# Kernel tuning notes

Measured on AMD Instinct MI355X. Metric: run time of the kernel, lower is better.

The kernel has to match this reference:

```python
import jax, jax.numpy as jnp
import numpy as np

EPS = 1e-5  # torch LayerNorm default


def _layernorm(x, g, b):
    mu = jnp.mean(x, axis=-1, keepdims=True)
    var = jnp.mean(jnp.square(x - mu), axis=-1, keepdims=True)
    return (x - mu) * jax.lax.rsqrt(var + EPS) * g + b


def _sparse_window_attn(x, wq, wk, wv, wo, span, stride, head_num):
    B, L, D = x.shape
    d = D // head_num  # dim_QK == dim_V == dim_q // head_num
    Q = (x @ wq.T).reshape(B, L, head_num, d).transpose(0, 2, 1, 3)  # [B,H,L,d]
    K = (x @ wk.T).reshape(B, L, head_num, d).transpose(0, 2, 1, 3)
    V = (x @ wv.T).reshape(B, L, head_num, d).transpose(0, 2, 1, 3)
    s = jnp.arange(span)
    i = jnp.arange(L)
    kvi = s[:, None] - (span - 1) + stride * i[None, :]       # [S,L] key index per (offset, query)
    valid = (kvi >= 0) & (kvi < L)
    kvic = jnp.clip(kvi, 0, L - 1)
    Kg = K[:, :, kvic, :]                                     # [B,H,S,L,d]
    scores = jnp.einsum('bhld,bhsld->bhsl', Q, Kg) / jnp.sqrt(jnp.float32(d))
    scores = jnp.where(valid[None, None], scores, -jnp.inf)
    p = jax.nn.softmax(scores, axis=2)                        # softmax over span (dim 2 in torch)
    Vg = V[:, :, kvic, :]                                     # [B,H,S,L,d]
    o = jnp.einsum('bhsl,bhsld->bhld', p, Vg)                 # invalid entries have p==0
    o = o.transpose(0, 2, 1, 3).reshape(B, L, D)
    return o @ wo.T


def setup_inputs() -> dict:
    key = jax.random.key(0)
    ks = jax.random.split(key, 8)
    B, L, D = 2, 2048, 512
    sc = 1.0 / np.sqrt(D)
    return {
        'query': jax.random.normal(ks[0], (B, L, D), jnp.float32),
        'ln_g': jnp.ones((D,), jnp.float32),
        'ln_b': jnp.zeros((D,), jnp.float32),
        'wq': jax.random.normal(ks[1], (D, D), jnp.float32) * sc,
        'wk': jax.random.normal(ks[2], (D, D), jnp.float32) * sc,
        'wv': jax.random.normal(ks[3], (D, D), jnp.float32) * sc,
        'wo': jax.random.normal(ks[4], (D, D), jnp.float32) * sc,
        'w1': jax.random.normal(ks[5], (2 * D, D), jnp.float32) * sc,
        'b1': jnp.zeros((2 * D,), jnp.float32),
        'w2': jax.random.normal(ks[6], (D, 2 * D), jnp.float32) * (1.0 / np.sqrt(2 * D)),
        'b2': jnp.zeros((D,), jnp.float32),
        'span': 64,
        'stride': 1,
        'head_num': 8,
    }


def reference(query, ln_g, ln_b, wq, wk, wv, wo, w1, b1, w2, b2, span, stride, head_num):
    # NOTE: the torch block applies the SAME LayerNorm (shared params) twice.
    x = _layernorm(query, ln_g, ln_b)
    x = _sparse_window_attn(x, wq, wk, wv, wo, span, stride, head_num)
    query = x + query
    x = _layernorm(query, ln_g, ln_b)
    x = jax.nn.gelu(x @ w1.T + b1, approximate=False) @ w2.T + b2
    return x + query
```

## Files before the change

kernel.cpp:

```cpp
#include <hip/hip_runtime.h>
#include <hip/hip_bf16.h>
#include <cmath>

typedef __bf16 bf16;
typedef __attribute__((ext_vector_type(8))) __bf16 bf16x8;
typedef __attribute__((ext_vector_type(4))) __bf16 bf16x4;
typedef __attribute__((ext_vector_type(4))) float f32x4;
typedef __attribute__((ext_vector_type(4))) unsigned int u32x4;

#define LD_B 2
#define LD_L 2048
#define LD_D 512
#define N_HEAD 8
#define HD 64
#define NTOK (LD_B * LD_L)

__device__ __forceinline__ void gload16(const void* g, void* l) {
  __builtin_amdgcn_global_load_lds(
      (const __attribute__((address_space(1))) void*)g,
      (__attribute__((address_space(3))) void*)l, 16, 0, 0);
}

__global__ __launch_bounds__(256) void cast6_kernel(
    const float* __restrict__ s0, const float* __restrict__ s1,
    const float* __restrict__ s2, const float* __restrict__ s3,
    const float* __restrict__ s4, const float* __restrict__ s5,
    bf16* __restrict__ d0, bf16* __restrict__ d1, bf16* __restrict__ d2,
    bf16* __restrict__ d3, bf16* __restrict__ d4, bf16* __restrict__ d5)
{
  int idx = blockIdx.x * 256 + threadIdx.x;
  const float* src; bf16* dst; int off;
  if (idx < 262144) {
    int seg = idx >> 16; off = idx & 65535;
    src = seg == 0 ? s0 : seg == 1 ? s1 : seg == 2 ? s2 : s3;
    dst = seg == 0 ? d0 : seg == 1 ? d1 : seg == 2 ? d2 : d3;
  } else {
    int t = idx - 262144;
    int seg = t >> 17; off = t & 131071;
    src = seg ? s5 : s4;
    dst = seg ? d5 : d4;
  }
  f32x4 v = ((const f32x4*)src)[off];
  bf16x4 o;
  o[0] = (bf16)v[0]; o[1] = (bf16)v[1]; o[2] = (bf16)v[2]; o[3] = (bf16)v[3];
  ((bf16x4*)dst)[off] = o;
}

__global__ __launch_bounds__(256) void ln_kernel(
    const float* __restrict__ x, const float* __restrict__ g,
    const float* __restrict__ b, bf16* __restrict__ out)
{
  const int wid = threadIdx.x >> 6, lane = threadIdx.x & 63;
  const int row = blockIdx.x * 4 + wid;
  const f32x4* xr = (const f32x4*)(x + (size_t)row * LD_D);
  f32x4 v0 = xr[lane * 2], v1 = xr[lane * 2 + 1];
  float s = v0[0] + v0[1] + v0[2] + v0[3] + v1[0] + v1[1] + v1[2] + v1[3];
#pragma unroll
  for (int off = 32; off; off >>= 1) s += __shfl_xor(s, off);
  const float mu = s * (1.f / 512.f);
  float vs = 0.f;
#pragma unroll
  for (int i = 0; i < 4; ++i) {
    float a0 = v0[i] - mu; vs += a0 * a0;
    float a1 = v1[i] - mu; vs += a1 * a1;
  }
#pragma unroll
  for (int off = 32; off; off >>= 1) vs += __shfl_xor(vs, off);
  const float rstd = rsqrtf(vs * (1.f / 512.f) + 1e-5f);
  const f32x4* gr = (const f32x4*)g;
  const f32x4* br = (const f32x4*)b;
  f32x4 g0 = gr[lane * 2], g1 = gr[lane * 2 + 1];
  f32x4 b0 = br[lane * 2], b1 = br[lane * 2 + 1];
  bf16x8 o;
#pragma unroll
  for (int i = 0; i < 4; ++i) o[i] = (bf16)((v0[i] - mu) * rstd * g0[i] + b0[i]);
#pragma unroll
  for (int i = 0; i < 4; ++i) o[i + 4] = (bf16)((v1[i] - mu) * rstd * g1[i] + b1[i]);
  *(bf16x8*)(&out[(size_t)row * LD_D + lane * 8]) = o;
}

template <int EPI>
__device__ __forceinline__ void gemm_core(
    const bf16* __restrict__ A, const bf16* __restrict__ Bw,
    int M, int N, int K,
    bf16* __restrict__ Cb, float* __restrict__ Cf,
    const float* __restrict__ bias, const float* __restrict__ res)
{
  __shared__ bf16 As[2][4096];
  __shared__ bf16 Bs[2][4096];
  const int tid = threadIdx.x;
  const int lane = tid & 63, wid = tid >> 6;
  const int wm = wid >> 1, wn = wid & 1;
  const int l15 = lane & 15, kg = lane >> 4;
  const int row0 = blockIdx.x * 64, col0 = blockIdx.y * 64;

  int srow[2], scol[2];
#pragma unroll
  for (int i = 0; i < 2; ++i) {
    int c = i * 256 + tid;
    srow[i] = c >> 3;
    scol[i] = ((c & 7) ^ (srow[i] & 7)) * 8;
  }

  f32x4 acc[2][2];
#pragma unroll
  for (int m = 0; m < 2; ++m)
#pragma unroll
    for (int n = 0; n < 2; ++n) acc[m][n] = (f32x4){0.f, 0.f, 0.f, 0.f};

  const int nt = K >> 6;
#define STAGE(buf, k0)                                                      \
  {                                                                         \
    _Pragma("unroll")                                                       \
    for (int i = 0; i < 2; ++i) {                                           \
      const bf16* ga = A + (size_t)(row0 + srow[i]) * K + (k0) + scol[i];   \
      const bf16* gb = Bw + (size_t)(col0 + srow[i]) * K + (k0) + scol[i];  \
      char* la = (char*)&As[buf][0] + (i * 4 + wid) * 1024;                 \
      char* lb = (char*)&Bs[buf][0] + (i * 4 + wid) * 1024;                 \
      gload16(ga, la);                                                      \
      gload16(gb, lb);                                                      \
    }                                                                       \
  }

  STAGE(0, 0);
  __syncthreads();
  for (int t = 0; t < nt; ++t) {
    if (t + 1 < nt) STAGE((t + 1) & 1, (t + 1) << 6);
    const char* pa = (const char*)&As[t & 1][0];
    const char* pb = (const char*)&Bs[t & 1][0];
#pragma unroll
    for (int kk = 0; kk < 2; ++kk) {
      bf16x8 af[2], bf[2];
#pragma unroll
      for (int m = 0; m < 2; ++m) {
        const int r = wm * 32 + m * 16 + l15;
        int off = r * 128 + kk * 64 + kg * 16;
        off ^= (r & 7) << 4;
        af[m] = *(const bf16x8*)(pa + off);
      }
#pragma unroll
      for (int n = 0; n < 2; ++n) {
        const int r = wn * 32 + n * 16 + l15;
        int off = r * 128 + kk * 64 + kg * 16;
        off ^= (r & 7) << 4;
        bf[n] = *(const bf16x8*)(pb + off);
      }
#pragma unroll
      for (int m = 0; m < 2; ++m)
#pragma unroll
        for (int n = 0; n < 2; ++n)
          acc[m][n] = __builtin_amdgcn_mfma_f32_16x16x32_bf16(af[m], bf[n], acc[m][n], 0, 0, 0);
    }
    __syncthreads();
  }
#undef STAGE

  const int orow = row0 + wm * 32, ocol = col0 + wn * 32;
#pragma unroll
  for (int m = 0; m < 2; ++m) {
#pragma unroll
    for (int n = 0; n < 2; ++n) {
#pragma unroll
      for (int e = 0; e < 4; ++e) {
        const int rr = orow + m * 16 + kg * 4 + e;
        const int cc = ocol + n * 16 + l15;
        const float v = acc[m][n][e];
        const size_t oi = (size_t)rr * N + cc;
        if constexpr (EPI == 0) {
          Cb[oi] = (bf16)v;
        } else if constexpr (EPI == 1) {
          Cf[oi] = v + res[oi];
        } else if constexpr (EPI == 2) {
          float t = v + bias[cc];
          Cb[oi] = (bf16)(0.5f * t * (1.f + erff(t * 0.70710678118654752f)));
        } else {
          Cf[oi] = v + bias[cc] + res[oi];
        }
      }
    }
  }
}

__global__ __launch_bounds__(256) void gemm_qkv_kernel(
    const bf16* __restrict__ A, const bf16* __restrict__ Wq,
    const bf16* __restrict__ Wk, const bf16* __restrict__ Wv,
    bf16* __restrict__ Qo, bf16* __restrict__ Ko, bf16* __restrict__ Vo)
{
  const bf16* W = blockIdx.z == 0 ? Wq : blockIdx.z == 1 ? Wk : Wv;
  bf16* O = blockIdx.z == 0 ? Qo : blockIdx.z == 1 ? Ko : Vo;
  gemm_core<0>(A, W, NTOK, 512, 512, O, nullptr, nullptr, nullptr);
}

template <int EPI>
__global__ __launch_bounds__(256) void gemm_kernel(
    const bf16* __restrict__ A, const bf16* __restrict__ Bw,
    int M, int N, int K, bf16* Cb, float* Cf,
    const float* __restrict__ bias, const float* __restrict__ res)
{
  gemm_core<EPI>(A, Bw, M, N, K, Cb, Cf, bias, res);
}

__global__ __launch_bounds__(256) void attn_kernel(
    const bf16* __restrict__ Qg, const bf16* __restrict__ Kg,
    const bf16* __restrict__ Vg, bf16* __restrict__ Og)
{
  constexpr int STK = 72;
  constexpr int STP = 136;
  __shared__ bf16 Ks[128][STK];
  __shared__ bf16 Qs[64][STK];
  __shared__ bf16 Vt[64][STP];
  __shared__ bf16 Ps[4][16][STP];
  const int tid = threadIdx.x;
  const int qt = blockIdx.x, bh = blockIdx.y;
  const int b = bh >> 3, h = bh & 7;
  const int q0 = qt * 64;
  const int j0 = q0 - 63;
  const size_t base = (size_t)b * LD_L * LD_D + h * HD;

  for (int c = tid; c < 128 * 8; c += 256) {
    const int r = c >> 3, d0 = (c & 7) * 8;
    const int j = j0 + r;
    u32x4 kv = (u32x4){0u, 0u, 0u, 0u};
    bf16x8 vv = (bf16x8)(__bf16)0.f;
    if (j >= 0 && j < LD_L) {
      kv = *(const u32x4*)(Kg + base + (size_t)j * LD_D + d0);
      vv = *(const bf16x8*)(Vg + base + (size_t)j * LD_D + d0);
    }
    *(u32x4*)(&Ks[r][d0]) = kv;
#pragma unroll
    for (int dd = 0; dd < 8; ++dd) Vt[d0 + dd][r] = vv[dd];
  }
  for (int c = tid; c < 64 * 8; c += 256) {
    const int r = c >> 3, d0 = (c & 7) * 8;
    *(u32x4*)(&Qs[r][d0]) =
        *(const u32x4*)(Qg + base + (size_t)(q0 + r) * LD_D + d0);
  }
  __syncthreads();

  const int lane = tid & 63, wid = tid >> 6;
  const int l15 = lane & 15, kg = lane >> 4;
  const int klo = 63 - q0;

  bf16x8 qf[2];
#pragma unroll
  for (int kk = 0; kk < 2; ++kk)
    qf[kk] = *(const bf16x8*)(&Qs[wid * 16 + l15][kk * 32 + kg * 8]);
  f32x4 s[8];
#pragma unroll
  for (int n = 0; n < 8; ++n) s[n] = (f32x4){0.f, 0.f, 0.f, 0.f};
#pragma unroll
  for (int kk = 0; kk < 2; ++kk)
#pragma unroll
    for (int n = 0; n < 8; ++n) {
      bf16x8 kf = *(const bf16x8*)(&Ks[n * 16 + l15][kk * 32 + kg * 8]);
      s[n] = __builtin_amdgcn_mfma_f32_16x16x32_bf16(qf[kk], kf, s[n], 0, 0, 0);
    }

  float p[8][4];
  float mx[4], sm[4];
#pragma unroll
  for (int e = 0; e < 4; ++e) { mx[e] = -INFINITY; sm[e] = 0.f; }
#pragma unroll
  for (int n = 0; n < 8; ++n) {
    const int k = n * 16 + l15;
#pragma unroll
    for (int e = 0; e < 4; ++e) {
      const int qi = wid * 16 + kg * 4 + e;
      const bool ok = (k >= qi) & (k <= qi + 63) & (k >= klo);
      float sv = ok ? s[n][e] * 0.125f : -INFINITY;
      p[n][e] = sv;
      mx[e] = fmaxf(mx[e], sv);
    }
  }
#pragma unroll
  for (int off = 8; off; off >>= 1)
#pragma unroll
    for (int e = 0; e < 4; ++e) mx[e] = fmaxf(mx[e], __shfl_xor(mx[e], off));
#pragma unroll
  for (int n = 0; n < 8; ++n)
#pragma unroll
    for (int e = 0; e < 4; ++e) {
      float pv = (p[n][e] == -INFINITY) ? 0.f : __expf(p[n][e] - mx[e]);
      p[n][e] = pv;
      sm[e] += pv;
    }
#pragma unroll
  for (int off = 8; off; off >>= 1)
#pragma unroll
    for (int e = 0; e < 4; ++e) sm[e] += __shfl_xor(sm[e], off);
  float rs[4];
#pragma unroll
  for (int e = 0; e < 4; ++e) rs[e] = 1.f / sm[e];

#pragma unroll
  for (int n = 0; n < 8; ++n)
#pragma unroll
    for (int e = 0; e < 4; ++e)
      Ps[wid][kg * 4 + e][n * 16 + l15] = (bf16)(p[n][e] * rs[e]);

  f32x4 o[4];
#pragma unroll
  for (int n = 0; n < 4; ++n) o[n] = (f32x4){0.f, 0.f, 0.f, 0.f};
#pragma unroll
  for (int ks = 0; ks < 4; ++ks) {
    bf16x8 pf = *(const bf16x8*)(&Ps[wid][l15][ks * 32 + kg * 8]);
#pragma unroll
    for (int n = 0; n < 4; ++n) {
      bf16x8 vf = *(const bf16x8*)(&Vt[n * 16 + l15][ks * 32 + kg * 8]);
      o[n] = __builtin_amdgcn_mfma_f32_16x16x32_bf16(pf, vf, o[n], 0, 0, 0);
    }
  }

  const int q = q0 + wid * 16 + kg * 4;
#pragma unroll
  for (int n = 0; n < 4; ++n)
#pragma unroll
    for (int e = 0; e < 4; ++e)
      Og[base + (size_t)(q + e) * LD_D + n * 16 + l15] = (bf16)o[n][e];
}

extern "C" void kernel_launch(void* const* d_in, const int* in_sizes, int n_in,
                              void* d_out, int out_size, void* d_ws, size_t ws_size,
                              hipStream_t stream)
{
  const float* query = (const float*)d_in[0];
  const float* ln_g = (const float*)d_in[1];
  const float* ln_b = (const float*)d_in[2];
  const float* wq = (const float*)d_in[3];
  const float* wk = (const float*)d_in[4];
  const float* wv = (const float*)d_in[5];
  const float* wo = (const float*)d_in[6];
  const float* w1 = (const float*)d_in[7];
  const float* b1 = (const float*)d_in[8];
  const float* w2 = (const float*)d_in[9];
  const float* b2 = (const float*)d_in[10];
  float* out = (float*)d_out;

  char* ws = (char*)d_ws;
  bf16* WQb = (bf16*)(ws + 0x000000);
  bf16* WKb = (bf16*)(ws + 0x080000);
  bf16* WVb = (bf16*)(ws + 0x100000);
  bf16* WOb = (bf16*)(ws + 0x180000);
  bf16* W1b = (bf16*)(ws + 0x200000);
  bf16* W2b = (bf16*)(ws + 0x300000);
  bf16* XLN = (bf16*)(ws + 0x400000);
  bf16* Qb  = (bf16*)(ws + 0x800000);
  bf16* Kb  = (bf16*)(ws + 0xC00000);
  bf16* Vb  = (bf16*)(ws + 0x1000000);
  bf16* ATb = (bf16*)(ws + 0x1400000);
  float* Q2 = (float*)(ws + 0x1800000);
  bf16* YLN = (bf16*)(ws + 0x2000000);
  bf16* Hb  = (bf16*)(ws + 0x2400000);

  cast6_kernel<<<2048, 256, 0, stream>>>(wq, wk, wv, wo, w1, w2,
                                         WQb, WKb, WVb, WOb, W1b, W2b);
  ln_kernel<<<1024, 256, 0, stream>>>(query, ln_g, ln_b, XLN);
  gemm_qkv_kernel<<<dim3(64, 8, 3), 256, 0, stream>>>(XLN, WQb, WKb, WVb, Qb, Kb, Vb);
  attn_kernel<<<dim3(32, 16), 256, 0, stream>>>(Qb, Kb, Vb, ATb);
  gemm_kernel<1><<<dim3(64, 8), 256, 0, stream>>>(ATb, WOb, NTOK, 512, 512,
                                                  nullptr, Q2, nullptr, query);
  ln_kernel<<<1024, 256, 0, stream>>>(Q2, ln_g, ln_b, YLN);
  gemm_kernel<2><<<dim3(64, 16), 256, 0, stream>>>(YLN, W1b, NTOK, 1024, 512,
                                                   Hb, nullptr, b1, nullptr);
  gemm_kernel<3><<<dim3(64, 8), 256, 0, stream>>>(Hb, W2b, NTOK, 512, 1024,
                                                  nullptr, out, b2, Q2);
}
```

Measured before the change: 152.5 us.

## Fuse QKV weights into one GEMM and enlarge GEMM tiles to 128

Concatenates Wq/Wk/Wv into a single 1536-wide weight so the QKV projection runs as one GEMM writing an interleaved QKV buffer, and the attention kernel reads Q/K/V from it with a 1536 row stride. The GEMM is templated on block tile size and all projections now use 128x128 or 128x64 tiles, raising data reuse per block at the cost of more registers and LDS and fewer blocks on a large GPU.

```diff
diff --git a/kernel.cpp b/kernel.cpp
--- a/kernel.cpp
+++ b/kernel.cpp
@@ -14,6 +14,7 @@
 #define N_HEAD 8
 #define HD 64
 #define NTOK (LD_B * LD_L)
+#define QKV_LD 1536
 
 __device__ __forceinline__ void gload16(const void* g, void* l) {
   __builtin_amdgcn_global_load_lds(
@@ -79,48 +80,59 @@
   *(bf16x8*)(&out[(size_t)row * LD_D + lane * 8]) = o;
 }
 
-template <int EPI>
-__device__ __forceinline__ void gemm_core(
+template <int BM, int BN, int EPI>
+__global__ __launch_bounds__(256) void gemm_kernel(
     const bf16* __restrict__ A, const bf16* __restrict__ Bw,
-    int M, int N, int K,
-    bf16* __restrict__ Cb, float* __restrict__ Cf,
+    int M, int N, int K, bf16* __restrict__ Cb, float* __restrict__ Cf,
     const float* __restrict__ bias, const float* __restrict__ res)
 {
-  __shared__ bf16 As[2][4096];
-  __shared__ bf16 Bs[2][4096];
+  constexpr int WM = BM / 2, WN = BN / 2;
+  constexpr int FM = WM / 16, FN = WN / 16;
+  constexpr int IA = BM / 32, IB = BN / 32;
+  __shared__ bf16 As[2][BM * 64];
+  __shared__ bf16 Bs[2][BN * 64];
   const int tid = threadIdx.x;
   const int lane = tid & 63, wid = tid >> 6;
   const int wm = wid >> 1, wn = wid & 1;
   const int l15 = lane & 15, kg = lane >> 4;
-  const int row0 = blockIdx.x * 64, col0 = blockIdx.y * 64;
-
-  int srow[2], scol[2];
-#pragma unroll
-  for (int i = 0; i < 2; ++i) {
+  const int row0 = blockIdx.x * BM, col0 = blockIdx.y * BN;
+
+  int srowA[IA], scolA[IA];
+#pragma unroll
+  for (int i = 0; i < IA; ++i) {
     int c = i * 256 + tid;
-    srow[i] = c >> 3;
-    scol[i] = ((c & 7) ^ (srow[i] & 7)) * 8;
-  }
-
-  f32x4 acc[2][2];
-#pragma unroll
-  for (int m = 0; m < 2; ++m)
-#pragma unroll
-    for (int n = 0; n < 2; ++n) acc[m][n] = (f32x4){0.f, 0.f, 0.f, 0.f};
+    srowA[i] = c >> 3;
+    scolA[i] = ((c & 7) ^ (srowA[i] & 7)) * 8;
+  }
+  int srowB[IB], scolB[IB];
+#pragma unroll
+  for (int i = 0; i < IB; ++i) {
+    int c = i * 256 + tid;
+    srowB[i] = c >> 3;
+    scolB[i] = ((c & 7) ^ (srowB[i] & 7)) * 8;
+  }
+
+  f32x4 acc[FM][FN];
+#pragma unroll
+  for (int m = 0; m < FM; ++m)
+#pragma unroll
+    for (int n = 0; n < FN; ++n) acc[m][n] = (f32x4){0.f, 0.f, 0.f, 0.f};
 
   const int nt = K >> 6;
-#define STAGE(buf, k0)                                                      \
-  {                                                                         \
-    _Pragma("unroll")                                                       \
-    for (int i = 0; i < 2; ++i) {                                           \
-      const bf16* ga = A + (size_t)(row0 + srow[i]) * K + (k0) + scol[i];   \
-      const bf16* gb = Bw + (size_t)(col0 + srow[i]) * K + (k0) + scol[i];  \
-      char* la = (char*)&As[buf][0] + (i * 4 + wid) * 1024;                 \
-      char* lb = (char*)&Bs[buf][0] + (i * 4 + wid) * 1024;                 \
-      gload16(ga, la);                                                      \
-      gload16(gb, lb);                                                      \
-    }                                                                       \
-  }
+  auto STAGE = [&](int buf, int k0) {
+#pragma unroll
+    for (int i = 0; i < IA; ++i) {
+      const bf16* ga = A + (size_t)(row0 + srowA[i]) * K + k0 + scolA[i];
+      char* la = (char*)&As[buf][0] + i * 4096 + wid * 1024;
+      gload16(ga, la);
+    }
+#pragma unroll
+    for (int i = 0; i < IB; ++i) {
+      const bf16* gb = Bw + (size_t)(col0 + srowB[i]) * K + k0 + scolB[i];
+      char* lb = (char*)&Bs[buf][0] + i * 4096 + wid * 1024;
+      gload16(gb, lb);
+    }
+  };
 
   STAGE(0, 0);
   __syncthreads();
@@ -130,36 +142,35 @@
     const char* pb = (const char*)&Bs[t & 1][0];
 #pragma unroll
     for (int kk = 0; kk < 2; ++kk) {
-      bf16x8 af[2], bf[2];
-#pragma unroll
-      for (int m = 0; m < 2; ++m) {
-        const int r = wm * 32 + m * 16 + l15;
+      bf16x8 af[FM], bf[FN];
+#pragma unroll
+      for (int m = 0; m < FM; ++m) {
+        const int r = wm * WM + m * 16 + l15;
         int off = r * 128 + kk * 64 + kg * 16;
         off ^= (r & 7) << 4;
         af[m] = *(const bf16x8*)(pa + off);
       }
 #pragma unroll
-      for (int n = 0; n < 2; ++n) {
-        const int r = wn * 32 + n * 16 + l15;
+      for (int n = 0; n < FN; ++n) {
+        const int r = wn * WN + n * 16 + l15;
         int off = r * 128 + kk * 64 + kg * 16;
         off ^= (r & 7) << 4;
         bf[n] = *(const bf16x8*)(pb + off);
       }
 #pragma unroll
-      for (int m = 0; m < 2; ++m)
-#pragma unroll
-        for (int n = 0; n < 2; ++n)
+      for (int m = 0; m < FM; ++m)
+#pragma unroll
+        for (int n = 0; n < FN; ++n)
           acc[m][n] = __builtin_amdgcn_mfma_f32_16x16x32_bf16(af[m], bf[n], acc[m][n], 0, 0, 0);
     }
     __syncthreads();
   }
-#undef STAGE
-
-  const int orow = row0 + wm * 32, ocol = col0 + wn * 32;
-#pragma unroll
-  for (int m = 0; m < 2; ++m) {
-#pragma unroll
-    for (int n = 0; n < 2; ++n) {
+
+  const int orow = row0 + wm * WM, ocol = col0 + wn * WN;
+#pragma unroll
+  for (int m = 0; m < FM; ++m) {
+#pragma unroll
+    for (int n = 0; n < FN; ++n) {
 #pragma unroll
       for (int e = 0; e < 4; ++e) {
         const int rr = orow + m * 16 + kg * 4 + e;
@@ -171,8 +182,8 @@
         } else if constexpr (EPI == 1) {
           Cf[oi] = v + res[oi];
         } else if constexpr (EPI == 2) {
-          float t = v + bias[cc];
-          Cb[oi] = (bf16)(0.5f * t * (1.f + erff(t * 0.70710678118654752f)));
+          float t2 = v + bias[cc];
+          Cb[oi] = (bf16)(0.5f * t2 * (1.f + erff(t2 * 0.70710678118654752f)));
         } else {
           Cf[oi] = v + bias[cc] + res[oi];
         }
@@ -181,28 +192,8 @@
   }
 }
 
-__global__ __launch_bounds__(256) void gemm_qkv_kernel(
-    const bf16* __restrict__ A, const bf16* __restrict__ Wq,
-    const bf16* __restrict__ Wk, const bf16* __restrict__ Wv,
-    bf16* __restrict__ Qo, bf16* __restrict__ Ko, bf16* __restrict__ Vo)
-{
-  const bf16* W = blockIdx.z == 0 ? Wq : blockIdx.z == 1 ? Wk : Wv;
-  bf16* O = blockIdx.z == 0 ? Qo : blockIdx.z == 1 ? Ko : Vo;
-  gemm_core<0>(A, W, NTOK, 512, 512, O, nullptr, nullptr, nullptr);
-}
-
-template <int EPI>
-__global__ __launch_bounds__(256) void gemm_kernel(
-    const bf16* __restrict__ A, const bf16* __restrict__ Bw,
-    int M, int N, int K, bf16* Cb, float* Cf,
-    const float* __restrict__ bias, const float* __restrict__ res)
-{
-  gemm_core<EPI>(A, Bw, M, N, K, Cb, Cf, bias, res);
-}
-
 __global__ __launch_bounds__(256) void attn_kernel(
-    const bf16* __restrict__ Qg, const bf16* __restrict__ Kg,
-    const bf16* __restrict__ Vg, bf16* __restrict__ Og)
+    const bf16* __restrict__ QKV, bf16* __restrict__ Og)
 {
   constexpr int STK = 72;
   constexpr int STP = 136;
@@ -215,7 +206,10 @@
   const int b = bh >> 3, h = bh & 7;
   const int q0 = qt * 64;
   const int j0 = q0 - 63;
-  const size_t base = (size_t)b * LD_L * LD_D + h * HD;
+  const size_t baseQ = (size_t)b * LD_L * QKV_LD + h * HD;
+  const size_t baseK = baseQ + 512;
+  const size_t baseV = baseQ + 1024;
+  const size_t baseO = (size_t)b * LD_L * LD_D + h * HD;
 
   for (int c = tid; c < 128 * 8; c += 256) {
     const int r = c >> 3, d0 = (c & 7) * 8;
@@ -223,8 +217,8 @@
     u32x4 kv = (u32x4){0u, 0u, 0u, 0u};
     bf16x8 vv = (bf16x8)(__bf16)0.f;
     if (j >= 0 && j < LD_L) {
-      kv = *(const u32x4*)(Kg + base + (size_t)j * LD_D + d0);
-      vv = *(const bf16x8*)(Vg + base + (size_t)j * LD_D + d0);
+      kv = *(const u32x4*)(QKV + baseK + (size_t)j * QKV_LD + d0);
+      vv = *(const bf16x8*)(QKV + baseV + (size_t)j * QKV_LD + d0);
     }
     *(u32x4*)(&Ks[r][d0]) = kv;
 #pragma unroll
@@ -233,7 +227,7 @@
   for (int c = tid; c < 64 * 8; c += 256) {
     const int r = c >> 3, d0 = (c & 7) * 8;
     *(u32x4*)(&Qs[r][d0]) =
-        *(const u32x4*)(Qg + base + (size_t)(q0 + r) * LD_D + d0);
+        *(const u32x4*)(QKV + baseQ + (size_t)(q0 + r) * QKV_LD + d0);
   }
   __syncthreads();
 
@@ -316,7 +310,7 @@
   for (int n = 0; n < 4; ++n)
 #pragma unroll
     for (int e = 0; e < 4; ++e)
-      Og[base + (size_t)(q + e) * LD_D + n * 16 + l15] = (bf16)o[n][e];
+      Og[baseO + (size_t)(q + e) * LD_D + n * 16 + l15] = (bf16)o[n][e];
 }
 
 extern "C" void kernel_launch(void* const* d_in, const int* in_sizes, int n_in,
@@ -337,31 +331,29 @@
   float* out = (float*)d_out;
 
   char* ws = (char*)d_ws;
-  bf16* WQb = (bf16*)(ws + 0x000000);
-  bf16* WKb = (bf16*)(ws + 0x080000);
-  bf16* WVb = (bf16*)(ws + 0x100000);
+  bf16* WQKVb = (bf16*)(ws + 0x000000);
   bf16* WOb = (bf16*)(ws + 0x180000);
   bf16* W1b = (bf16*)(ws + 0x200000);
   bf16* W2b = (bf16*)(ws + 0x300000);
   bf16* XLN = (bf16*)(ws + 0x400000);
-  bf16* Qb  = (bf16*)(ws + 0x800000);
-  bf16* Kb  = (bf16*)(ws + 0xC00000);
-  bf16* Vb  = (bf16*)(ws + 0x1000000);
+  bf16* QKVb = (bf16*)(ws + 0x800000);
   bf16* ATb = (bf16*)(ws + 0x1400000);
   float* Q2 = (float*)(ws + 0x1800000);
   bf16* YLN = (bf16*)(ws + 0x2000000);
-  bf16* Hb  = (bf16*)(ws + 0x2400000);
-
-  cast6_kernel<<<2048, 256, 0, stream>>>(wq, wk, wv, wo, w1, w2,
-                                         WQb, WKb, WVb, WOb, W1b, W2b);
+  bf16* Hb = (bf16*)(ws + 0x2400000);
+
+  cast6_kernel<<<2048, 256, 0, stream>>>(
+      wq, wk, wv, wo, w1, w2,
+      WQKVb, WQKVb + 262144, WQKVb + 524288, WOb, W1b, W2b);
   ln_kernel<<<1024, 256, 0, stream>>>(query, ln_g, ln_b, XLN);
-  gemm_qkv_kernel<<<dim3(64, 8, 3), 256, 0, stream>>>(XLN, WQb, WKb, WVb, Qb, Kb, Vb);
-  attn_kernel<<<dim3(32, 16), 256, 0, stream>>>(Qb, Kb, Vb, ATb);
-  gemm_kernel<1><<<dim3(64, 8), 256, 0, stream>>>(ATb, WOb, NTOK, 512, 512,
-                                                  nullptr, Q2, nullptr, query);
+  gemm_kernel<128, 128, 0><<<dim3(32, 12), 256, 0, stream>>>(
+      XLN, WQKVb, NTOK, QKV_LD, 512, QKVb, nullptr, nullptr, nullptr);
+  attn_kernel<<<dim3(32, 16), 256, 0, stream>>>(QKVb, ATb);
+  gemm_kernel<128, 64, 1><<<dim3(32, 8), 256, 0, stream>>>(
+      ATb, WOb, NTOK, 512, 512, nullptr, Q2, nullptr, query);
   ln_kernel<<<1024, 256, 0, stream>>>(Q2, ln_g, ln_b, YLN);
-  gemm_kernel<2><<<dim3(64, 16), 256, 0, stream>>>(YLN, W1b, NTOK, 1024, 512,
-                                                   Hb, nullptr, b1, nullptr);
-  gemm_kernel<3><<<dim3(64, 8), 256, 0, stream>>>(Hb, W2b, NTOK, 512, 1024,
-                                                  nullptr, out, b2, Q2);
-}
+  gemm_kernel<128, 128, 2><<<dim3(32, 8), 256, 0, stream>>>(
+      YLN, W1b, NTOK, 1024, 512, Hb, nullptr, b1, nullptr);
+  gemm_kernel<128, 64, 3><<<dim3(32, 8), 256, 0, stream>>>(
+      Hb, W2b, NTOK, 512, 1024, nullptr, out, b2, Q2);
+}
```

Measured after the change: 161.8 us. 1.06x slower.

## Fuse weight cast with first LayerNorm and pack QKV into one GEMM

Applied to the files above, without the earlier changes.

Merges the weight-cast kernel and the first LayerNorm into a single prep kernel whose blocks are split by index, saving one launch. The Q, K and V weights are written contiguously so one GEMM with N=1536 produces an interleaved QKV buffer. The attention kernel now reads Q, K and V from that buffer with a row stride of 1536. This removes a launch and the per-block weight selection, at the cost of strided reads in attention.

```diff
diff --git a/kernel.cpp b/kernel.cpp
--- a/kernel.cpp
+++ b/kernel.cpp
@@ -14,6 +14,7 @@
 #define N_HEAD 8
 #define HD 64
 #define NTOK (LD_B * LD_L)
+#define QKV_LD 1536
 
 __device__ __forceinline__ void gload16(const void* g, void* l) {
   __builtin_amdgcn_global_load_lds(
@@ -21,35 +22,34 @@
       (__attribute__((address_space(3))) void*)l, 16, 0, 0);
 }
 
-__global__ __launch_bounds__(256) void cast6_kernel(
+__global__ __launch_bounds__(256) void prep_kernel(
+    const float* __restrict__ x, const float* __restrict__ g,
+    const float* __restrict__ b, bf16* __restrict__ xln,
     const float* __restrict__ s0, const float* __restrict__ s1,
     const float* __restrict__ s2, const float* __restrict__ s3,
     const float* __restrict__ s4, const float* __restrict__ s5,
     bf16* __restrict__ d0, bf16* __restrict__ d1, bf16* __restrict__ d2,
     bf16* __restrict__ d3, bf16* __restrict__ d4, bf16* __restrict__ d5)
 {
-  int idx = blockIdx.x * 256 + threadIdx.x;
-  const float* src; bf16* dst; int off;
-  if (idx < 262144) {
-    int seg = idx >> 16; off = idx & 65535;
-    src = seg == 0 ? s0 : seg == 1 ? s1 : seg == 2 ? s2 : s3;
-    dst = seg == 0 ? d0 : seg == 1 ? d1 : seg == 2 ? d2 : d3;
-  } else {
-    int t = idx - 262144;
-    int seg = t >> 17; off = t & 131071;
-    src = seg ? s5 : s4;
-    dst = seg ? d5 : d4;
-  }
-  f32x4 v = ((const f32x4*)src)[off];
-  bf16x4 o;
-  o[0] = (bf16)v[0]; o[1] = (bf16)v[1]; o[2] = (bf16)v[2]; o[3] = (bf16)v[3];
-  ((bf16x4*)dst)[off] = o;
-}
-
-__global__ __launch_bounds__(256) void ln_kernel(
-    const float* __restrict__ x, const float* __restrict__ g,
-    const float* __restrict__ b, bf16* __restrict__ out)
-{
+  if (blockIdx.x >= 1024) {
+    int idx = (blockIdx.x - 1024) * 256 + threadIdx.x;
+    const float* src; bf16* dst; int off;
+    if (idx < 262144) {
+      int seg = idx >> 16; off = idx & 65535;
+      src = seg == 0 ? s0 : seg == 1 ? s1 : seg == 2 ? s2 : s3;
+      dst = seg == 0 ? d0 : seg == 1 ? d1 : seg == 2 ? d2 : d3;
+    } else {
+      int t = idx - 262144;
+      int seg = t >> 17; off = t & 131071;
+      src = seg ? s5 : s4;
+      dst = seg ? d5 : d4;
+    }
+    f32x4 v = ((const f32x4*)src)[off];
+    bf16x4 o;
+    o[0] = (bf16)v[0]; o[1] = (bf16)v[1]; o[2] = (bf16)v[2]; o[3] = (bf16)v[3];
+    ((bf16x4*)dst)[off] = o;
+    return;
+  }
   const int wid = threadIdx.x >> 6, lane = threadIdx.x & 63;
   const int row = blockIdx.x * 4 + wid;
   const f32x4* xr = (const f32x4*)(x + (size_t)row * LD_D);
@@ -76,14 +76,46 @@
   for (int i = 0; i < 4; ++i) o[i] = (bf16)((v0[i] - mu) * rstd * g0[i] + b0[i]);
 #pragma unroll
   for (int i = 0; i < 4; ++i) o[i + 4] = (bf16)((v1[i] - mu) * rstd * g1[i] + b1[i]);
+  *(bf16x8*)(&xln[(size_t)row * LD_D + lane * 8]) = o;
+}
+
+__global__ __launch_bounds__(256) void ln_kernel(
+    const float* __restrict__ x, const float* __restrict__ g,
+    const float* __restrict__ b, bf16* __restrict__ out)
+{
+  const int wid = threadIdx.x >> 6, lane = threadIdx.x & 63;
+  const int row = blockIdx.x * 4 + wid;
+  const f32x4* xr = (const f32x4*)(x + (size_t)row * LD_D);
+  f32x4 v0 = xr[lane * 2], v1 = xr[lane * 2 + 1];
+  float s = v0[0] + v0[1] + v0[2] + v0[3] + v1[0] + v1[1] + v1[2] + v1[3];
+#pragma unroll
+  for (int off = 32; off; off >>= 1) s += __shfl_xor(s, off);
+  const float mu = s * (1.f / 512.f);
+  float vs = 0.f;
+#pragma unroll
+  for (int i = 0; i < 4; ++i) {
+    float a0 = v0[i] - mu; vs += a0 * a0;
+    float a1 = v1[i] - mu; vs += a1 * a1;
+  }
+#pragma unroll
+  for (int off = 32; off; off >>= 1) vs += __shfl_xor(vs, off);
+  const float rstd = rsqrtf(vs * (1.f / 512.f) + 1e-5f);
+  const f32x4* gr = (const f32x4*)g;
+  const f32x4* br = (const f32x4*)b;
+  f32x4 g0 = gr[lane * 2], g1 = gr[lane * 2 + 1];
+  f32x4 b0 = br[lane * 2], b1 = br[lane * 2 + 1];
+  bf16x8 o;
+#pragma unroll
+  for (int i = 0; i < 4; ++i) o[i] = (bf16)((v0[i] - mu) * rstd * g0[i] + b0[i]);
+#pragma unroll
+  for (int i = 0; i < 4; ++i) o[i + 4] = (bf16)((v1[i] - mu) * rstd * g1[i] + b1[i]);
   *(bf16x8*)(&out[(size_t)row * LD_D + lane * 8]) = o;
 }
 
 template <int EPI>
-__device__ __forceinline__ void gemm_core(
+__global__ __launch_bounds__(256) void gemm_kernel(
     const bf16* __restrict__ A, const bf16* __restrict__ Bw,
-    int M, int N, int K,
-    bf16* __restrict__ Cb, float* __restrict__ Cf,
+    int M, int N, int K, bf16* __restrict__ Cb, float* __restrict__ Cf,
     const float* __restrict__ bias, const float* __restrict__ res)
 {
   __shared__ bf16 As[2][4096];
@@ -171,8 +203,8 @@
         } else if constexpr (EPI == 1) {
           Cf[oi] = v + res[oi];
         } else if constexpr (EPI == 2) {
-          float t = v + bias[cc];
-          Cb[oi] = (bf16)(0.5f * t * (1.f + erff(t * 0.70710678118654752f)));
+          float t2 = v + bias[cc];
+          Cb[oi] = (bf16)(0.5f * t2 * (1.f + erff(t2 * 0.70710678118654752f)));
         } else {
           Cf[oi] = v + bias[cc] + res[oi];
         }
@@ -181,28 +213,8 @@
   }
 }
 
-__global__ __launch_bounds__(256) void gemm_qkv_kernel(
-    const bf16* __restrict__ A, const bf16* __restrict__ Wq,
-    const bf16* __restrict__ Wk, const bf16* __restrict__ Wv,
-    bf16* __restrict__ Qo, bf16* __restrict__ Ko, bf16* __restrict__ Vo)
-{
-  const bf16* W = blockIdx.z == 0 ? Wq : blockIdx.z == 1 ? Wk : Wv;
-  bf16* O = blockIdx.z == 0 ? Qo : blockIdx.z == 1 ? Ko : Vo;
-  gemm_core<0>(A, W, NTOK, 512, 512, O, nullptr, nullptr, nullptr);
-}
-
-template <int EPI>
-__global__ __launch_bounds__(256) void gemm_kernel(
-    const bf16* __restrict__ A, const bf16* __restrict__ Bw,
-    int M, int N, int K, bf16* Cb, float* Cf,
-    const float* __restrict__ bias, const float* __restrict__ res)
-{
-  gemm_core<EPI>(A, Bw, M, N, K, Cb, Cf, bias, res);
-}
-
 __global__ __launch_bounds__(256) void attn_kernel(
-    const bf16* __restrict__ Qg, const bf16* __restrict__ Kg,
-    const bf16* __restrict__ Vg, bf16* __restrict__ Og)
+    const bf16* __restrict__ QKV, bf16* __restrict__ Og)
 {
   constexpr int STK = 72;
   constexpr int STP = 136;
@@ -215,7 +227,10 @@
   const int b = bh >> 3, h = bh & 7;
   const int q0 = qt * 64;
   const int j0 = q0 - 63;
-  const size_t base = (size_t)b * LD_L * LD_D + h * HD;
+  const size_t baseQ = (size_t)b * LD_L * QKV_LD + h * HD;
+  const size_t baseK = baseQ + 512;
+  const size_t baseV = baseQ + 1024;
+  const size_t baseO = (size_t)b * LD_L * LD_D + h * HD;
 
   for (int c = tid; c < 128 * 8; c += 256) {
     const int r = c >> 3, d0 = (c & 7) * 8;
@@ -223,8 +238,8 @@
     u32x4 kv = (u32x4){0u, 0u, 0u, 0u};
     bf16x8 vv = (bf16x8)(__bf16)0.f;
     if (j >= 0 && j < LD_L) {
-      kv = *(const u32x4*)(Kg + base + (size_t)j * LD_D + d0);
-      vv = *(const bf16x8*)(Vg + base + (size_t)j * LD_D + d0);
+      kv = *(const u32x4*)(QKV + baseK + (size_t)j * QKV_LD + d0);
+      vv = *(const bf16x8*)(QKV + baseV + (size_t)j * QKV_LD + d0);
     }
     *(u32x4*)(&Ks[r][d0]) = kv;
 #pragma unroll
@@ -233,7 +248,7 @@
   for (int c = tid; c < 64 * 8; c += 256) {
     const int r = c >> 3, d0 = (c & 7) * 8;
     *(u32x4*)(&Qs[r][d0]) =
-        *(const u32x4*)(Qg + base + (size_t)(q0 + r) * LD_D + d0);
+        *(const u32x4*)(QKV + baseQ + (size_t)(q0 + r) * QKV_LD + d0);
   }
   __syncthreads();
 
@@ -316,7 +331,7 @@
   for (int n = 0; n < 4; ++n)
 #pragma unroll
     for (int e = 0; e < 4; ++e)
-      Og[base + (size_t)(q + e) * LD_D + n * 16 + l15] = (bf16)o[n][e];
+      Og[baseO + (size_t)(q + e) * LD_D + n * 16 + l15] = (bf16)o[n][e];
 }
 
 extern "C" void kernel_launch(void* const* d_in, const int* in_sizes, int n_in,
@@ -337,31 +352,29 @@
   float* out = (float*)d_out;
 
   char* ws = (char*)d_ws;
-  bf16* WQb = (bf16*)(ws + 0x000000);
-  bf16* WKb = (bf16*)(ws + 0x080000);
-  bf16* WVb = (bf16*)(ws + 0x100000);
+  bf16* WQKVb = (bf16*)(ws + 0x000000);
   bf16* WOb = (bf16*)(ws + 0x180000);
   bf16* W1b = (bf16*)(ws + 0x200000);
   bf16* W2b = (bf16*)(ws + 0x300000);
   bf16* XLN = (bf16*)(ws + 0x400000);
-  bf16* Qb  = (bf16*)(ws + 0x800000);
-  bf16* Kb  = (bf16*)(ws + 0xC00000);
-  bf16* Vb  = (bf16*)(ws + 0x1000000);
+  bf16* QKVb = (bf16*)(ws + 0x800000);
   bf16* ATb = (bf16*)(ws + 0x1400000);
   float* Q2 = (float*)(ws + 0x1800000);
   bf16* YLN = (bf16*)(ws + 0x2000000);
-  bf16* Hb  = (bf16*)(ws + 0x2400000);
-
-  cast6_kernel<<<2048, 256, 0, stream>>>(wq, wk, wv, wo, w1, w2,
-                                         WQb, WKb, WVb, WOb, W1b, W2b);
-  ln_kernel<<<1024, 256, 0, stream>>>(query, ln_g, ln_b, XLN);
-  gemm_qkv_kernel<<<dim3(64, 8, 3), 256, 0, stream>>>(XLN, WQb, WKb, WVb, Qb, Kb, Vb);
-  attn_kernel<<<dim3(32, 16), 256, 0, stream>>>(Qb, Kb, Vb, ATb);
-  gemm_kernel<1><<<dim3(64, 8), 256, 0, stream>>>(ATb, WOb, NTOK, 512, 512,
-                                                  nullptr, Q2, nullptr, query);
+  bf16* Hb = (bf16*)(ws + 0x2400000);
+
+  prep_kernel<<<3072, 256, 0, stream>>>(
+      query, ln_g, ln_b, XLN,
+      wq, wk, wv, wo, w1, w2,
+      WQKVb, WQKVb + 262144, WQKVb + 524288, WOb, W1b, W2b);
+  gemm_kernel<0><<<dim3(64, 24), 256, 0, stream>>>(
+      XLN, WQKVb, NTOK, QKV_LD, 512, QKVb, nullptr, nullptr, nullptr);
+  attn_kernel<<<dim3(32, 16), 256, 0, stream>>>(QKVb, ATb);
+  gemm_kernel<1><<<dim3(64, 8), 256, 0, stream>>>(
+      ATb, WOb, NTOK, 512, 512, nullptr, Q2, nullptr, query);
   ln_kernel<<<1024, 256, 0, stream>>>(Q2, ln_g, ln_b, YLN);
-  gemm_kernel<2><<<dim3(64, 16), 256, 0, stream>>>(YLN, W1b, NTOK, 1024, 512,
-                                                   Hb, nullptr, b1, nullptr);
-  gemm_kernel<3><<<dim3(64, 8), 256, 0, stream>>>(Hb, W2b, NTOK, 512, 1024,
-                                                  nullptr, out, b2, Q2);
-}
+  gemm_kernel<2><<<dim3(64, 16), 256, 0, stream>>>(
+      YLN, W1b, NTOK, 1024, 512, Hb, nullptr, b1, nullptr);
+  gemm_kernel<3><<<dim3(64, 8), 256, 0, stream>>>(
+      Hb, W2b, NTOK, 512, 1024, nullptr, out, b2, Q2);
+}
```

New measurement: 149.8 us. Within noise of the previous version (-1.8%).
